# Optimization experiments

Hardware: AMD Instinct MI355X
Metric: run time of the kernel (lower is better)

## Reference

```python
import jax, jax.numpy as jnp
import numpy as np

EPS = 1e-6  # torch F.pairwise_distance eps, added to the difference elementwise

B, Z = 8192, 128
N_CLASSES = 62
P = int(N_CLASSES * 1.5)  # 93 proxies


def pdist(a, b):
    """||a_i - b_j + EPS||_2 for all pairs, without a [N,M,Z] intermediate.
    Expansion: ||a-b||^2 + 2*EPS*sum(a-b) + Z*EPS^2."""
    aa = jnp.sum(a * a, axis=-1)[:, None]
    bb = jnp.sum(b * b, axis=-1)[None, :]
    ab = a @ b.T
    eps_term = 2.0 * EPS * (jnp.sum(a, -1)[:, None] - jnp.sum(b, -1)[None, :]) + a.shape[-1] * EPS * EPS
    return jnp.sqrt(jnp.maximum(aa + bb - 2.0 * ab + eps_term, 0.0))


def setup_inputs() -> dict:
    key = jax.random.key(0)
    k0, k1, k2 = jax.random.split(key, 3)
    z = jax.random.normal(k0, (B, Z), dtype=jnp.float32)
    y_idx = jax.random.randint(k1, (B,), 0, N_CLASSES, dtype=jnp.int32)
    proxies = jax.random.uniform(k2, (P, Z), dtype=jnp.float32)  # nn.init.uniform_
    y_map = jnp.arange(N_CLASSES, dtype=jnp.int32)  # y_to_relative_y_train (unique classes)
    return {"z": z, "y_idx": y_idx, "proxies": proxies, "y_map": y_map}


def reference(z, y_idx, proxies, y_map):
    # F.normalize(proxies, p=2, dim=-1) with 1e-12 clamp
    prx = proxies / jnp.maximum(jnp.linalg.norm(proxies, axis=-1, keepdims=True), 1e-12)
    # y_rel[j] = position where y_to_relative_y_train == y_idx[j] (exactly one match)
    y_rel = jnp.argmax(y_map[None, :] == y_idx[:, None], axis=-1)  # [B]

    anchors = np.arange(0, z.shape[0] - 3, 3)  # static anchor indices i
    z_a = z[anchors]                            # [A,Z]

    # nearest proxy to each anchor
    D_prox = pdist(z_a, prx)                    # [A,P]
    prox_p = prx[jnp.argmin(D_prox, axis=-1)]   # [A,Z]

    # distance from chosen proxy to every sample; restrict to suffix j>=i with same class
    D_pz = pdist(prox_p, z)                     # [A,B]
    mask = (np.arange(z.shape[0])[None, :] >= anchors[:, None]) & \
           (y_rel[None, :] == y_rel[anchors][:, None])  # [A,B], row i always has j=i True
    D_pos = jnp.where(mask, D_pz, -jnp.inf)
    j_p = jnp.argmax(D_pos, axis=-1)            # hardest positive index
    D_p = jnp.take_along_axis(D_pos, j_p[:, None], axis=-1)[:, 0]  # [A]

    # distances from hardest positive to all proxies -> NCA denominator
    D_n = pdist(z[j_p], prx)                    # [A,P]
    losses = D_p + jax.nn.logsumexp(-D_n, axis=-1)  # -log(exp(-D_p)/sum exp(-D_n))
    return jnp.mean(losses)
```

## Files before the change

### kernel.cpp

```cpp
#include <hip/hip_runtime.h>
#include <math.h>

#define B_N   8192
#define Z_D   128
#define P_N   93
#define NCLS  62
#define A_N   2730
#define BCAP  256
#define GT_S  96
#define NPART 683
#define TWO_EPS   2e-6f
#define ZEPS2     (128.0f * 1e-6f * 1e-6f)

#define AT_LD(p)      __hip_atomic_load((p), __ATOMIC_RELAXED, __HIP_MEMORY_SCOPE_AGENT)
#define AT_ST(p, v)   __hip_atomic_store((p), (v), __ATOMIC_RELAXED, __HIP_MEMORY_SCOPE_AGENT)
#define AT_ADDU(p, v) __hip_atomic_fetch_add((p), (v), __ATOMIC_RELAXED, __HIP_MEMORY_SCOPE_AGENT)

__device__ __forceinline__ float wave_sum(float v) {
#pragma unroll
  for (int off = 1; off < 64; off <<= 1) v += __shfl_xor(v, off, 64);
  return v;
}
__device__ __forceinline__ float wave_min(float v) {
#pragma unroll
  for (int off = 1; off < 64; off <<= 1) v = fminf(v, __shfl_xor(v, off, 64));
  return v;
}

__global__ __launch_bounds__(512) void kA(
    const float* __restrict__ z, const int* __restrict__ y_idx,
    const float* __restrict__ prox, const int* __restrict__ y_map,
    float* __restrict__ pp, float* __restrict__ sp,
    float* __restrict__ zz, float* __restrict__ sz,
    int* __restrict__ cnt, int2* __restrict__ bkt, float* __restrict__ GT,
    unsigned int* __restrict__ ctr) {
  __shared__ float linv[6];
  __shared__ int lmem[BCAP];
  __shared__ int lcnt;
  const int b = blockIdx.x, tid = threadIdx.x;
  const int lane = tid & 63, wv = tid >> 6;

  if (b == 0 && tid < 17) ctr[tid * 32] = 0u;

  if (b < 256) {
    const int jch = b & 15, kt = b >> 4, k0 = kt * 6;
    const int nk = (kt == 15) ? 3 : 6;
    const int j = jch * 512 + tid;
    const float* __restrict__ zrow = z + (size_t)j * Z_D;
    if (wv < nk) {
      const int k = k0 + wv;
      const float a = prox[k * Z_D + lane];
      const float c = prox[k * Z_D + 64 + lane];
      const float s = wave_sum(a + c);
      const float q = wave_sum(a * a + c * c);
      const float inv = 1.0f / fmaxf(sqrtf(q), 1e-12f);
      if (lane == 0) {
        linv[wv] = inv;
        if (jch == 0) { pp[k] = q * inv * inv; sp[k] = s * inv; }
      }
    }
    __syncthreads();
    if (kt < 15) {
      const float* __restrict__ p0 = prox + (size_t)(k0 + 0) * Z_D;
      const float* __restrict__ p1 = prox + (size_t)(k0 + 1) * Z_D;
      const float* __restrict__ p2 = prox + (size_t)(k0 + 2) * Z_D;
      const float* __restrict__ p3 = prox + (size_t)(k0 + 3) * Z_D;
      const float* __restrict__ p4 = prox + (size_t)(k0 + 4) * Z_D;
      const float* __restrict__ p5 = prox + (size_t)(k0 + 5) * Z_D;
      float a0 = 0, a1 = 0, a2 = 0, a3 = 0, a4 = 0, a5 = 0;
#pragma unroll 8
      for (int i4 = 0; i4 < Z_D; i4 += 4) {
        const float4 zv = *(const float4*)(zrow + i4);
        const float4 q0 = *(const float4*)(p0 + i4);
        const float4 q1 = *(const float4*)(p1 + i4);
        const float4 q2 = *(const float4*)(p2 + i4);
        const float4 q3 = *(const float4*)(p3 + i4);
        const float4 q4 = *(const float4*)(p4 + i4);
        const float4 q5 = *(const float4*)(p5 + i4);
        a0 += zv.x * q0.x + zv.y * q0.y + zv.z * q0.z + zv.w * q0.w;
        a1 += zv.x * q1.x + zv.y * q1.y + zv.z * q1.z + zv.w * q1.w;
        a2 += zv.x * q2.x + zv.y * q2.y + zv.z * q2.z + zv.w * q2.w;
        a3 += zv.x * q3.x + zv.y * q3.y + zv.z * q3.z + zv.w * q3.w;
        a4 += zv.x * q4.x + zv.y * q4.y + zv.z * q4.z + zv.w * q4.w;
        a5 += zv.x * q5.x + zv.y * q5.y + zv.z * q5.z + zv.w * q5.w;
      }
      const float v0 = linv[0], v1 = linv[1], v2 = linv[2];
      const float v3 = linv[3], v4 = linv[4], v5 = linv[5];
      float* g = GT + (size_t)j * GT_S + k0;
      *(float2*)(g + 0) = make_float2(a0 * v0, a1 * v1);
      *(float2*)(g + 2) = make_float2(a2 * v2, a3 * v3);
      *(float2*)(g + 4) = make_float2(a4 * v4, a5 * v5);
    } else {
      const float* __restrict__ p0 = prox + (size_t)90 * Z_D;
      const float* __restrict__ p1 = prox + (size_t)91 * Z_D;
      const float* __restrict__ p2 = prox + (size_t)92 * Z_D;
      float a0 = 0, a1 = 0, a2 = 0, zs = 0, zq = 0;
#pragma unroll 8
      for (int i4 = 0; i4 < Z_D; i4 += 4) {
        const float4 zv = *(const float4*)(zrow + i4);
        const float4 q0 = *(const float4*)(p0 + i4);
        const float4 q1 = *(const float4*)(p1 + i4);
        const float4 q2 = *(const float4*)(p2 + i4);
        zs += zv.x + zv.y + zv.z + zv.w;
        zq += zv.x * zv.x + zv.y * zv.y + zv.z * zv.z + zv.w * zv.w;
        a0 += zv.x * q0.x + zv.y * q0.y + zv.z * q0.z + zv.w * q0.w;
        a1 += zv.x * q1.x + zv.y * q1.y + zv.z * q1.z + zv.w * q1.w;
        a2 += zv.x * q2.x + zv.y * q2.y + zv.z * q2.z + zv.w * q2.w;
      }
      float* g = GT + (size_t)j * GT_S + 90;
      *(float2*)(g) = make_float2(a0 * linv[0], a1 * linv[1]);
      g[2] = a2 * linv[2];
      zz[j] = zq;
      sz[j] = zs;
    }
  } else {
    const int c = b - 256;
    if (tid == 0) lcnt = 0;
    __syncthreads();
    const int ym = y_map[c];
    for (int j = tid; j < B_N; j += 512) {
      if (y_idx[j] == ym) {
        const int pos = atomicAdd(&lcnt, 1);
        if (pos < BCAP) lmem[pos] = j;
      }
    }
    __syncthreads();
    const int n = min(lcnt, BCAP);
    if (tid == 0) cnt[c] = n;
    for (int m = wv; m < n; m += 8) {
      const int j = lmem[m];
      const float a = z[(size_t)j * Z_D + lane];
      const float c2 = z[(size_t)j * Z_D + 64 + lane];
      const float s = wave_sum(a + c2);
      const float q = wave_sum(a * a + c2 * c2);
      if (lane == 0)
        bkt[c * BCAP + m] = make_int2(j, __float_as_int(q - TWO_EPS * s));
    }
  }
}

__global__ __launch_bounds__(256) void kB2(
    const int* __restrict__ y_idx, const int* __restrict__ y_map,
    const float* __restrict__ pp, const float* __restrict__ sp,
    const float* __restrict__ zz, const float* __restrict__ sz,
    const int* __restrict__ cnt, const int2* __restrict__ bkt,
    const float* __restrict__ GT, float* partial, unsigned int* ctr,
    float* __restrict__ out) {
  __shared__ float lpp[P_N], lsp[P_N];
  __shared__ int lymap[NCLS];
  __shared__ float part[4];
  const int b = blockIdx.x;
  const int tid = threadIdx.x, lane = tid & 63, wv = tid >> 6;
  if (tid < P_N) { lpp[tid] = pp[tid]; lsp[tid] = sp[tid]; }
  if (tid < NCLS) lymap[tid] = y_map[tid];
  __syncthreads();

  const int wid = b * 4 + wv;
  float loss = 0.0f;
  if (wid < A_N) {
    const int i = 3 * wid;
    const int yi = y_idx[i];
    const unsigned long long mm = __ballot(lane < NCLS && lymap[lane] == yi);
    const int cls = __ffsll(mm) - 1;
    const float zzi = zz[i], szi = sz[i];
    const int kB = lane + 64;

    const float* __restrict__ GTi = GT + (size_t)i * GT_S;
    float v1 = fmaxf(zzi + lpp[lane] - 2.0f * GTi[lane] +
                     TWO_EPS * (szi - lsp[lane]) + ZEPS2, 0.0f);
    int i1 = lane;
    if (kB < P_N) {
      const float v2 = fmaxf(zzi + lpp[kB] - 2.0f * GTi[kB] +
                             TWO_EPS * (szi - lsp[kB]) + ZEPS2, 0.0f);
      if (v2 < v1) { v1 = v2; i1 = kB; }
    }
#pragma unroll
    for (int off = 1; off < 64; off <<= 1) {
      const float ov = __shfl_xor(v1, off, 64);
      const int oi = __shfl_xor(i1, off, 64);
      if (ov < v1 || (ov == v1 && oi < i1)) { v1 = ov; i1 = oi; }
    }
    const int p = i1;

    const float cp = lpp[p] + TWO_EPS * lsp[p] + ZEPS2;
    const int n = cnt[cls];
    const int2* __restrict__ bk = bkt + cls * BCAP;
    float best = -INFINITY;
    int bestj = 0x7fffffff;
    for (int t = lane; t < n; t += 64) {
      const int2 e = bk[t];
      const int jj = e.x;
      if (jj >= i) {
        const float vv = fmaxf(cp + __int_as_float(e.y) -
                               2.0f * GT[(size_t)jj * GT_S + p], 0.0f);
        if (vv > best || (vv == best && jj < bestj)) { best = vv; bestj = jj; }
      }
    }
#pragma unroll
    for (int off = 1; off < 64; off <<= 1) {
      const float ov = __shfl_xor(best, off, 64);
      const int oj = __shfl_xor(bestj, off, 64);
      if (ov > best || (ov == best && oj < bestj)) { best = ov; bestj = oj; }
    }
    const float Dp = sqrtf(best);
    const int jp = bestj;

    const float zzj = zz[jp], szj = sz[jp];
    const float* __restrict__ GTj = GT + (size_t)jp * GT_S;
    const float d1 = sqrtf(fmaxf(zzj + lpp[lane] - 2.0f * GTj[lane] +
                                 TWO_EPS * (szj - lsp[lane]) + ZEPS2, 0.0f));
    float d2 = INFINITY;
    if (kB < P_N)
      d2 = sqrtf(fmaxf(zzj + lpp[kB] - 2.0f * GTj[kB] +
                       TWO_EPS * (szj - lsp[kB]) + ZEPS2, 0.0f));
    const float mn = wave_min(fminf(d1, d2));
    float ss = expf(mn - d1) + ((kB < P_N) ? expf(mn - d2) : 0.0f);
    ss = wave_sum(ss);
    loss = Dp - mn + logf(ss);
  }
  if (lane == 0) part[wv] = (wid < A_N) ? loss : 0.0f;
  __syncthreads();

  if (wv == 0) {
    int last = 0;
    if (lane == 0) {
      AT_ST(&partial[b], part[0] + part[1] + part[2] + part[3]);
      __builtin_amdgcn_s_waitcnt(0);
      const int sub = b & 15;
      const unsigned quota = (sub < 11) ? 43u : 42u;
      const unsigned old = AT_ADDU(&ctr[sub * 32], 1u);
      if (old == quota - 1u) {
        const unsigned so = AT_ADDU(&ctr[16 * 32], 1u);
        if (so == 15u) last = 1;
      }
    }
    last = __shfl(last, 0, 64);
    if (last) {
      float s = 0.0f;
#pragma unroll
      for (int r = 0; r < 11; ++r) {
        const int t = lane + r * 64;
        if (t < NPART) s += AT_LD(&partial[t]);
      }
      s = wave_sum(s);
      if (lane == 0) out[0] = s * (1.0f / (float)A_N);
    }
  }
}

extern "C" void kernel_launch(void* const* d_in, const int* in_sizes, int n_in,
                              void* d_out, int out_size, void* d_ws, size_t ws_size,
                              hipStream_t stream) {
  const float* z = (const float*)d_in[0];
  const int* y_idx = (const int*)d_in[1];
  const float* prox = (const float*)d_in[2];
  const int* y_map = (const int*)d_in[3];
  float* out = (float*)d_out;

  char* ws = (char*)d_ws;
  unsigned int* ctr = (unsigned int*)(ws + 0);
  float* pp    = (float*)(ws + 2560);
  float* sp    = (float*)(ws + 3072);
  float* zz    = (float*)(ws + 3584);
  float* sz    = (float*)(ws + 36352);
  int*   cnt   = (int*)  (ws + 69120);
  int2*  bkt   = (int2*) (ws + 69376);
  float* parts = (float*)(ws + 196352);
  float* GT    = (float*)(ws + 199168);

  kA<<<256 + NCLS, 512, 0, stream>>>(z, y_idx, prox, y_map,
                                     pp, sp, zz, sz, cnt, bkt, GT, ctr);
  kB2<<<NPART, 256, 0, stream>>>(y_idx, y_map, pp, sp, zz, sz,
                                 cnt, bkt, GT, parts, ctr, out);
}
```

Baseline: 90.60 us.

## Stage normalized proxies in LDS and slim class buckets to index-only

The GEMM blocks now load their six proxy rows once into shared memory, pre-scaled by the inverse norm, instead of every thread re-reading them from global memory and scaling afterwards. The per-class bucket blocks no longer recompute row norms of z. They only store sample indices. The norm-minus-eps term is instead written per sample as a new w array by the tail GEMM blocks and gathered in the second kernel. This removes redundant global loads and the wave reductions in the bucket blocks, at the cost of an extra barrier and one extra indirect gather per candidate.

```diff
diff --git a/kernel.cpp b/kernel.cpp
--- a/kernel.cpp
+++ b/kernel.cpp
@@ -31,11 +31,11 @@
     const float* __restrict__ z, const int* __restrict__ y_idx,
     const float* __restrict__ prox, const int* __restrict__ y_map,
     float* __restrict__ pp, float* __restrict__ sp,
-    float* __restrict__ zz, float* __restrict__ sz,
-    int* __restrict__ cnt, int2* __restrict__ bkt, float* __restrict__ GT,
+    float* __restrict__ zz, float* __restrict__ sz, float* __restrict__ w,
+    int* __restrict__ cnt, int* __restrict__ bkt, float* __restrict__ GT,
     unsigned int* __restrict__ ctr) {
   __shared__ float linv[6];
-  __shared__ int lmem[BCAP];
+  __shared__ float pt[6 * Z_D];
   __shared__ int lcnt;
   const int b = blockIdx.x, tid = threadIdx.x;
   const int lane = tid & 63, wv = tid >> 6;
@@ -60,23 +60,28 @@
       }
     }
     __syncthreads();
+    {
+      const int nf = nk * 32;
+      const float4* __restrict__ src = (const float4*)(prox + (size_t)k0 * Z_D);
+      for (int t = tid; t < nf; t += 512) {
+        const float iv = linv[t >> 5];
+        const float4 v = src[t];
+        ((float4*)pt)[t] = make_float4(v.x * iv, v.y * iv, v.z * iv, v.w * iv);
+      }
+    }
+    __syncthreads();
     if (kt < 15) {
-      const float* __restrict__ p0 = prox + (size_t)(k0 + 0) * Z_D;
-      const float* __restrict__ p1 = prox + (size_t)(k0 + 1) * Z_D;
-      const float* __restrict__ p2 = prox + (size_t)(k0 + 2) * Z_D;
-      const float* __restrict__ p3 = prox + (size_t)(k0 + 3) * Z_D;
-      const float* __restrict__ p4 = prox + (size_t)(k0 + 4) * Z_D;
-      const float* __restrict__ p5 = prox + (size_t)(k0 + 5) * Z_D;
       float a0 = 0, a1 = 0, a2 = 0, a3 = 0, a4 = 0, a5 = 0;
 #pragma unroll 8
       for (int i4 = 0; i4 < Z_D; i4 += 4) {
         const float4 zv = *(const float4*)(zrow + i4);
-        const float4 q0 = *(const float4*)(p0 + i4);
-        const float4 q1 = *(const float4*)(p1 + i4);
-        const float4 q2 = *(const float4*)(p2 + i4);
-        const float4 q3 = *(const float4*)(p3 + i4);
-        const float4 q4 = *(const float4*)(p4 + i4);
-        const float4 q5 = *(const float4*)(p5 + i4);
+        const int f = i4 >> 2;
+        const float4 q0 = ((const float4*)pt)[0 * 32 + f];
+        const float4 q1 = ((const float4*)pt)[1 * 32 + f];
+        const float4 q2 = ((const float4*)pt)[2 * 32 + f];
+        const float4 q3 = ((const float4*)pt)[3 * 32 + f];
+        const float4 q4 = ((const float4*)pt)[4 * 32 + f];
+        const float4 q5 = ((const float4*)pt)[5 * 32 + f];
         a0 += zv.x * q0.x + zv.y * q0.y + zv.z * q0.z + zv.w * q0.w;
         a1 += zv.x * q1.x + zv.y * q1.y + zv.z * q1.z + zv.w * q1.w;
         a2 += zv.x * q2.x + zv.y * q2.y + zv.z * q2.z + zv.w * q2.w;
@@ -84,23 +89,19 @@
         a4 += zv.x * q4.x + zv.y * q4.y + zv.z * q4.z + zv.w * q4.w;
         a5 += zv.x * q5.x + zv.y * q5.y + zv.z * q5.z + zv.w * q5.w;
       }
-      const float v0 = linv[0], v1 = linv[1], v2 = linv[2];
-      const float v3 = linv[3], v4 = linv[4], v5 = linv[5];
       float* g = GT + (size_t)j * GT_S + k0;
-      *(float2*)(g + 0) = make_float2(a0 * v0, a1 * v1);
-      *(float2*)(g + 2) = make_float2(a2 * v2, a3 * v3);
-      *(float2*)(g + 4) = make_float2(a4 * v4, a5 * v5);
+      *(float2*)(g + 0) = make_float2(a0, a1);
+      *(float2*)(g + 2) = make_float2(a2, a3);
+      *(float2*)(g + 4) = make_float2(a4, a5);
     } else {
-      const float* __restrict__ p0 = prox + (size_t)90 * Z_D;
-      const float* __restrict__ p1 = prox + (size_t)91 * Z_D;
-      const float* __restrict__ p2 = prox + (size_t)92 * Z_D;
       float a0 = 0, a1 = 0, a2 = 0, zs = 0, zq = 0;
 #pragma unroll 8
       for (int i4 = 0; i4 < Z_D; i4 += 4) {
         const float4 zv = *(const float4*)(zrow + i4);
-        const float4 q0 = *(const float4*)(p0 + i4);
-        const float4 q1 = *(const float4*)(p1 + i4);
-        const float4 q2 = *(const float4*)(p2 + i4);
+        const int f = i4 >> 2;
+        const float4 q0 = ((const float4*)pt)[0 * 32 + f];
+        const float4 q1 = ((const float4*)pt)[1 * 32 + f];
+        const float4 q2 = ((const float4*)pt)[2 * 32 + f];
         zs += zv.x + zv.y + zv.z + zv.w;
         zq += zv.x * zv.x + zv.y * zv.y + zv.z * zv.z + zv.w * zv.w;
         a0 += zv.x * q0.x + zv.y * q0.y + zv.z * q0.z + zv.w * q0.w;
@@ -108,10 +109,11 @@
         a2 += zv.x * q2.x + zv.y * q2.y + zv.z * q2.z + zv.w * q2.w;
       }
       float* g = GT + (size_t)j * GT_S + 90;
-      *(float2*)(g) = make_float2(a0 * linv[0], a1 * linv[1]);
-      g[2] = a2 * linv[2];
+      *(float2*)(g) = make_float2(a0, a1);
+      g[2] = a2;
       zz[j] = zq;
       sz[j] = zs;
+      w[j] = zq - TWO_EPS * zs;
     }
   } else {
     const int c = b - 256;
@@ -121,21 +123,11 @@
     for (int j = tid; j < B_N; j += 512) {
       if (y_idx[j] == ym) {
         const int pos = atomicAdd(&lcnt, 1);
-        if (pos < BCAP) lmem[pos] = j;
-      }
-    }
-    __syncthreads();
-    const int n = min(lcnt, BCAP);
-    if (tid == 0) cnt[c] = n;
-    for (int m = wv; m < n; m += 8) {
-      const int j = lmem[m];
-      const float a = z[(size_t)j * Z_D + lane];
-      const float c2 = z[(size_t)j * Z_D + 64 + lane];
-      const float s = wave_sum(a + c2);
-      const float q = wave_sum(a * a + c2 * c2);
-      if (lane == 0)
-        bkt[c * BCAP + m] = make_int2(j, __float_as_int(q - TWO_EPS * s));
-    }
+        if (pos < BCAP) bkt[c * BCAP + pos] = j;
+      }
+    }
+    __syncthreads();
+    if (tid == 0) cnt[c] = min(lcnt, BCAP);
   }
 }
 
@@ -143,7 +135,8 @@
     const int* __restrict__ y_idx, const int* __restrict__ y_map,
     const float* __restrict__ pp, const float* __restrict__ sp,
     const float* __restrict__ zz, const float* __restrict__ sz,
-    const int* __restrict__ cnt, const int2* __restrict__ bkt,
+    const float* __restrict__ w,
+    const int* __restrict__ cnt, const int* __restrict__ bkt,
     const float* __restrict__ GT, float* partial, unsigned int* ctr,
     float* __restrict__ out) {
   __shared__ float lpp[P_N], lsp[P_N];
@@ -184,15 +177,13 @@
 
     const float cp = lpp[p] + TWO_EPS * lsp[p] + ZEPS2;
     const int n = cnt[cls];
-    const int2* __restrict__ bk = bkt + cls * BCAP;
+    const int* __restrict__ bk = bkt + cls * BCAP;
     float best = -INFINITY;
     int bestj = 0x7fffffff;
     for (int t = lane; t < n; t += 64) {
-      const int2 e = bk[t];
-      const int jj = e.x;
+      const int jj = bk[t];
       if (jj >= i) {
-        const float vv = fmaxf(cp + __int_as_float(e.y) -
-                               2.0f * GT[(size_t)jj * GT_S + p], 0.0f);
+        const float vv = fmaxf(cp + w[jj] - 2.0f * GT[(size_t)jj * GT_S + p], 0.0f);
         if (vv > best || (vv == best && jj < bestj)) { best = vv; bestj = jj; }
       }
     }
@@ -263,13 +254,14 @@
   float* sp    = (float*)(ws + 3072);
   float* zz    = (float*)(ws + 3584);
   float* sz    = (float*)(ws + 36352);
-  int*   cnt   = (int*)  (ws + 69120);
-  int2*  bkt   = (int2*) (ws + 69376);
-  float* parts = (float*)(ws + 196352);
-  float* GT    = (float*)(ws + 199168);
+  float* w     = (float*)(ws + 69120);
+  int*   cnt   = (int*)  (ws + 101888);
+  int*   bkt   = (int*)  (ws + 102144);
+  float* parts = (float*)(ws + 165632);
+  float* GT    = (float*)(ws + 168448);
 
   kA<<<256 + NCLS, 512, 0, stream>>>(z, y_idx, prox, y_map,
-                                     pp, sp, zz, sz, cnt, bkt, GT, ctr);
-  kB2<<<NPART, 256, 0, stream>>>(y_idx, y_map, pp, sp, zz, sz,
+                                     pp, sp, zz, sz, w, cnt, bkt, GT, ctr);
+  kB2<<<NPART, 256, 0, stream>>>(y_idx, y_map, pp, sp, zz, sz, w,
                                  cnt, bkt, GT, parts, ctr, out);
 }
```

After: 81.44 us. 1.11x faster.
